# Kernel tuning notes

Hardware: AMD Instinct MI355X
Metric: run time of the kernel (lower is better)

Reference implementation:

```python
import jax, jax.numpy as jnp
import numpy as np

B, C, H, W = 32, 256, 32, 32   # batch, hidden_dim, latent grid
D, K = 256, 4096               # embedding_dim, num_embeddings
COMMITMENT_COST = 0.25


def setup_inputs() -> dict:
    key = jax.random.key(0)
    k1, k2, k3 = jax.random.split(key, 3)
    x = jax.random.normal(k1, (B, C, H, W), dtype=jnp.float32)
    conv_w = jax.random.normal(k2, (D, C), dtype=jnp.float32) * 0.02  # 1x1 conv kernel
    conv_b = jnp.zeros((D,), dtype=jnp.float32)
    # torch init: uniform_(-1/num_embeddings, 1/num_embeddings)
    emb = jax.random.uniform(k3, (K, D), dtype=jnp.float32,
                             minval=-1.0 / K, maxval=1.0 / K)
    return {"x": x, "conv_w": conv_w, "conv_b": conv_b, "emb": emb}


def reference(x, conv_w, conv_b, emb):
    # pre_vq_conv1: 1x1 conv == per-pixel matmul
    z = jnp.einsum('bchw,dc->bdhw', x, conv_w) + conv_b[None, :, None, None]
    inputs = jnp.transpose(z, (0, 2, 3, 1))            # [B,H,W,D]
    flat = inputs.reshape(-1, D)                       # [N,D]
    dist = (jnp.sum(flat * flat, axis=1, keepdims=True)
            + jnp.sum(emb * emb, axis=1)
            - 2.0 * flat @ emb.T)                      # [N,K]
    idx = jnp.argmin(dist, axis=1)                     # [N]
    # one-hot @ emb == direct gather
    quantized = emb[idx].reshape(inputs.shape)         # [B,H,W,D]
    sg = jax.lax.stop_gradient
    e_latent_loss = jnp.mean((sg(quantized) - inputs) ** 2)
    q_latent_loss = jnp.mean((quantized - sg(inputs)) ** 2)
    loss = q_latent_loss + COMMITMENT_COST * e_latent_loss
    # straight-through estimator
    quantized_st = inputs + sg(quantized - inputs)
    quantized_out = jnp.transpose(quantized_st, (0, 3, 1, 2))  # [B,D,H,W]
    # perplexity: mean one-hot == normalized code counts
    n = flat.shape[0]
    avg_probs = jnp.zeros((K,), dtype=jnp.float32).at[idx].add(1.0) / n
    perplexity = jnp.exp(-jnp.sum(avg_probs * jnp.log(avg_probs + 1e-10)))
    return quantized_out, loss, perplexity
```

## Files before the change

kernel.cpp:

```cpp
#include <hip/hip_runtime.h>
#include <math.h>

#define BB   32
#define CC   256
#define HH   32
#define WW   32
#define DD   256
#define KK   4096
#define HW   1024
#define NPIX 32768
#define NELE 8388608
#define EPS_REPAIR 1e-5f

typedef unsigned short ushort_t;
typedef __attribute__((ext_vector_type(8))) short short8;
typedef __attribute__((ext_vector_type(4))) float f32x4;

__device__ __forceinline__ unsigned short f2bf(float v) {
    union { float f; unsigned u; } c; c.f = v;
    unsigned r = c.u + 0x7FFFu + ((c.u >> 16) & 1u);
    return (unsigned short)(r >> 16);
}
__device__ __forceinline__ float bf2f(unsigned short b) {
    union { unsigned u; float f; } c; c.u = ((unsigned)b) << 16;
    return c.f;
}
__device__ __forceinline__ void gll16(const void* g, void* l) {
    __builtin_amdgcn_global_load_lds(
        (const __attribute__((address_space(1))) void*)g,
        (__attribute__((address_space(3))) void*)l, 16, 0, 0);
}

__global__ void k_zero(int* __restrict__ counts, float* __restrict__ accum) {
    int i = blockIdx.x * 256 + threadIdx.x;
    if (i < KK) counts[i] = 0;
    if (i < 2)  accum[i]  = 0.0f;
}

__global__ void k_packB(const float* __restrict__ emb, ushort_t* __restrict__ Bp,
                        float* __restrict__ e_norm) {
    int k = blockIdx.x;
    int lane = threadIdx.x;
    float4 v = reinterpret_cast<const float4*>(emb + (size_t)k * DD)[lane];
    float s = v.x * v.x + v.y * v.y + v.z * v.z + v.w * v.w;
    float vv[4] = {v.x, v.y, v.z, v.w};
    ushort_t* row = Bp + (size_t)k * 768 + lane * 4;
    #pragma unroll
    for (int c = 0; c < 4; ++c) {
        unsigned short h = f2bf(vv[c]);
        unsigned short l = f2bf(vv[c] - bf2f(h));
        row[c] = h; row[256 + c] = h; row[512 + c] = l;
    }
    #pragma unroll
    for (int off = 32; off; off >>= 1) s += __shfl_down(s, off);
    if (lane == 0) e_norm[k] = s;
}

__global__ __launch_bounds__(256) void k_conv(const float* __restrict__ x,
                                              const float* __restrict__ w,
                                              const float* __restrict__ bias,
                                              ushort_t* __restrict__ A2) {
    __shared__ __align__(16) float xt[32][260];
    int t = threadIdx.x;
    int n0 = blockIdx.x * 32;
    int b = n0 >> 10, hw0 = n0 & 1023;
    const float* xb = x + (size_t)b * (CC * HW) + hw0;

    int p = t & 31, cg = t >> 5;
    #pragma unroll
    for (int it = 0; it < 32; ++it) {
        int c = it * 8 + cg;
        xt[p][c] = xb[c * HW + p];
    }
    __syncthreads();

    int d = t;
    float acc[32];
    float bv = bias[d];
    #pragma unroll
    for (int i = 0; i < 32; ++i) acc[i] = bv;

    const float4* wrow = reinterpret_cast<const float4*>(w + (size_t)d * CC);
    for (int c4 = 0; c4 < 64; ++c4) {
        float4 w4 = wrow[c4];
        #pragma unroll
        for (int pp = 0; pp < 32; ++pp) {
            float4 x4 = *reinterpret_cast<const float4*>(&xt[pp][c4 * 4]);
            acc[pp] = fmaf(w4.x, x4.x, acc[pp]);
            acc[pp] = fmaf(w4.y, x4.y, acc[pp]);
            acc[pp] = fmaf(w4.z, x4.z, acc[pp]);
            acc[pp] = fmaf(w4.w, x4.w, acc[pp]);
        }
    }
    #pragma unroll
    for (int pp = 0; pp < 32; ++pp) {
        float v = acc[pp];
        unsigned short h = f2bf(v);
        unsigned short l = f2bf(v - bf2f(h));
        ushort_t* arow = A2 + (size_t)(n0 + pp) * 512;
        arow[d] = h; arow[256 + d] = l;
    }
}

__global__ __launch_bounds__(256, 2) void k_mfma_top2(
    const ushort_t* __restrict__ A2,
    const ushort_t* __restrict__ Bp,
    const float* __restrict__ e_norm,
    float* __restrict__ tv1, int* __restrict__ ti1,
    float* __restrict__ tv2, int* __restrict__ ti2) {
    __shared__ __align__(16) short As[128][64];
    __shared__ __align__(16) short Bs[128][64];
    __shared__ float mgv[128][2][2];
    __shared__ int   mgi[128][2][2];

    const int t  = threadIdx.x;
    const int mb = blockIdx.x >> 2, ch = blockIdx.x & 3;
    const int n0 = mb * 128, c0 = ch * 1024;
    const int w  = t >> 6, lane = t & 63;
    const int wr = w >> 1, wc = w & 1;
    const int lr = lane & 15, lg = lane >> 4;

    const int srow = t >> 3;
    const int scol = (t & 7) * 8;

    float v1[4][4], v2r[4][4];
    int   i1[4][4], i2r[4][4];
    #pragma unroll
    for (int m = 0; m < 4; ++m)
        #pragma unroll
        for (int j = 0; j < 4; ++j) {
            v1[m][j] = 3.0e38f; v2r[m][j] = 3.0e38f;
            i1[m][j] = 0x7FFFFFFF; i2r[m][j] = 0x7FFFFFFF;
        }

    for (int sub = 0; sub < 8; ++sub) {
        const int code0 = c0 + sub * 128;
        f32x4 acc[4][4];
        const f32x4 vz = {0.f, 0.f, 0.f, 0.f};
        #pragma unroll
        for (int m = 0; m < 4; ++m)
            #pragma unroll
            for (int n = 0; n < 4; ++n) acc[m][n] = vz;

        for (int ks = 0; ks < 12; ++ks) {
            const int Acol = (ks < 8) ? ks * 64 : (ks - 8) * 64;
            const int Bcol = ks * 64;
            __syncthreads();
            #pragma unroll
            for (int s = 0; s < 4; ++s) {
                const int r = srow + 32 * s;
                gll16(&A2[(size_t)(n0 + r) * 512 + Acol + scol], &As[r][scol]);
                gll16(&Bp[(size_t)(code0 + r) * 768 + Bcol + scol], &Bs[r][scol]);
            }
            __syncthreads();
            #pragma unroll
            for (int kk = 0; kk < 2; ++kk) {
                short8 a[4], b[4];
                #pragma unroll
                for (int m = 0; m < 4; ++m)
                    a[m] = *reinterpret_cast<const short8*>(
                        &As[wr * 64 + m * 16 + lr][kk * 32 + lg * 8]);
                #pragma unroll
                for (int n = 0; n < 4; ++n)
                    b[n] = *reinterpret_cast<const short8*>(
                        &Bs[wc * 64 + n * 16 + lr][kk * 32 + lg * 8]);
                #pragma unroll
                for (int m = 0; m < 4; ++m)
                    #pragma unroll
                    for (int n = 0; n < 4; ++n)
                        acc[m][n] = __builtin_amdgcn_mfma_f32_16x16x32_bf16(
                            a[m], b[n], acc[m][n], 0, 0, 0);
            }
        }
        #pragma unroll
        for (int n = 0; n < 4; ++n) {
            const int col = code0 + wc * 64 + n * 16 + lr;
            const float en = e_norm[col];
            #pragma unroll
            for (int m = 0; m < 4; ++m)
                #pragma unroll
                for (int j = 0; j < 4; ++j) {
                    const float s = fmaf(-2.0f, acc[m][n][j], en);
                    const bool b1 = s < v1[m][j];
                    const bool b2 = s < v2r[m][j];
                    v2r[m][j] = b1 ? v1[m][j] : (b2 ? s : v2r[m][j]);
                    i2r[m][j] = b1 ? i1[m][j] : (b2 ? col : i2r[m][j]);
                    v1[m][j]  = b1 ? s   : v1[m][j];
                    i1[m][j]  = b1 ? col : i1[m][j];
                }
        }
    }

    #pragma unroll
    for (int mask = 1; mask <= 8; mask <<= 1) {
        #pragma unroll
        for (int m = 0; m < 4; ++m)
            #pragma unroll
            for (int j = 0; j < 4; ++j) {
                const float ov1 = __shfl_xor(v1[m][j], mask);
                const int   oi1 = __shfl_xor(i1[m][j], mask);
                const float ov2 = __shfl_xor(v2r[m][j], mask);
                const int   oi2 = __shfl_xor(i2r[m][j], mask);
                const bool tb = (ov1 < v1[m][j]) || (ov1 == v1[m][j] && oi1 < i1[m][j]);
                const float w1 = tb ? ov1 : v1[m][j];  const int w1i = tb ? oi1 : i1[m][j];
                const float l1 = tb ? v1[m][j] : ov1;  const int l1i = tb ? i1[m][j] : oi1;
                const float c2 = tb ? ov2 : v2r[m][j]; const int c2i = tb ? oi2 : i2r[m][j];
                const bool t2b = (c2 < l1) || (c2 == l1 && c2i < l1i);
                v1[m][j] = w1; i1[m][j] = w1i;
                v2r[m][j] = t2b ? c2 : l1; i2r[m][j] = t2b ? c2i : l1i;
            }
    }
    if (lr == 0) {
        #pragma unroll
        for (int m = 0; m < 4; ++m)
            #pragma unroll
            for (int j = 0; j < 4; ++j) {
                const int r = wr * 64 + m * 16 + lg * 4 + j;
                mgv[r][wc][0] = v1[m][j];  mgv[r][wc][1] = v2r[m][j];
                mgi[r][wc][0] = i1[m][j];  mgi[r][wc][1] = i2r[m][j];
            }
    }
    __syncthreads();
    if (t < 128) {
        const float a1 = mgv[t][0][0], a2 = mgv[t][0][1];
        const int  ai1 = mgi[t][0][0], ai2 = mgi[t][0][1];
        const float b1 = mgv[t][1][0], b2 = mgv[t][1][1];
        const int  bi1 = mgi[t][1][0], bi2 = mgi[t][1][1];
        const bool tb = (b1 < a1) || (b1 == a1 && bi1 < ai1);
        const float w1 = tb ? b1 : a1;  const int w1i = tb ? bi1 : ai1;
        const float l1 = tb ? a1 : b1;  const int l1i = tb ? ai1 : bi1;
        const float c2 = tb ? b2 : a2;  const int c2i = tb ? bi2 : ai2;
        const bool t2b = (c2 < l1) || (c2 == l1 && c2i < l1i);
        const size_t o = (size_t)ch * NPIX + n0 + t;
        tv1[o] = w1; ti1[o] = w1i;
        tv2[o] = t2b ? c2 : l1; ti2[o] = t2b ? c2i : l1i;
    }
}

__global__ __launch_bounds__(256) void k_select(
    const float* __restrict__ tv1, const int* __restrict__ ti1,
    const float* __restrict__ tv2, const int* __restrict__ ti2,
    const ushort_t* __restrict__ A2, const float* __restrict__ emb,
    const float* __restrict__ e_norm, int* __restrict__ idx) {
    const int n = blockIdx.x * 256 + threadIdx.x;
    float g1 = tv1[n], g2 = tv2[n];
    int  gi1 = ti1[n], gi2 = ti2[n];
    #pragma unroll
    for (int c = 1; c < 4; ++c) {
        const size_t o = (size_t)c * NPIX + n;
        const float b1 = tv1[o], b2 = tv2[o];
        const int  bi1 = ti1[o], bi2 = ti2[o];
        const bool tb = (b1 < g1) || (b1 == g1 && bi1 < gi1);
        const float w1 = tb ? b1 : g1;  const int w1i = tb ? bi1 : gi1;
        const float l1 = tb ? g1 : b1;  const int l1i = tb ? gi1 : bi1;
        const float c2 = tb ? b2 : g2;  const int c2i = tb ? bi2 : gi2;
        const bool t2b = (c2 < l1) || (c2 == l1 && c2i < l1i);
        g1 = w1; gi1 = w1i;
        g2 = t2b ? c2 : l1; gi2 = t2b ? c2i : l1i;
    }
    int best = gi1;
    if (g2 - g1 < EPS_REPAIR) {
        const ushort_t* za = A2 + (size_t)n * 512;
        const float* e1 = emb + (size_t)gi1 * DD;
        const float* e2 = emb + (size_t)gi2 * DD;
        float d1 = 0.f, d2 = 0.f;
        for (int d = 0; d < DD; ++d) {
            const float z = bf2f(za[d]) + bf2f(za[256 + d]);
            d1 = fmaf(z, e1[d], d1);
            d2 = fmaf(z, e2[d], d2);
        }
        const float s1 = e_norm[gi1] - 2.f * d1;
        const float s2 = e_norm[gi2] - 2.f * d2;
        best = (s2 < s1 || (s2 == s1 && gi2 < gi1)) ? gi2 : gi1;
    }
    idx[n] = best;
}

__global__ __launch_bounds__(256) void k_gather(const float* __restrict__ emb,
                                                const ushort_t* __restrict__ A2,
                                                const int* __restrict__ idx,
                                                float* __restrict__ out,
                                                float* __restrict__ accum) {
    __shared__ float qt[256][33];
    int t = threadIdx.x;
    int n0 = blockIdx.x * 32;
    int b = n0 >> 10, hw0 = n0 & 1023;

    float ss = 0.0f;
    for (int p = 0; p < 32; ++p) {
        int row = idx[n0 + p];
        float q = emb[(size_t)row * DD + t];
        const ushort_t* za = A2 + (size_t)(n0 + p) * 512;
        float z = bf2f(za[t]) + bf2f(za[256 + t]);
        float df = q - z;
        ss = fmaf(df, df, ss);
        qt[t][p] = q;
    }
    __syncthreads();

    int dg = t >> 5, p = t & 31;
    float* ob = out + (size_t)b * (DD * HW) + hw0;
    #pragma unroll
    for (int s = 0; s < 32; ++s) {
        int d = dg + 8 * s;
        ob[d * HW + p] = qt[d][p];
    }

    #pragma unroll
    for (int off = 32; off; off >>= 1) ss += __shfl_down(ss, off);
    __shared__ float wsum[4];
    if ((t & 63) == 0) wsum[t >> 6] = ss;
    __syncthreads();
    if (t == 0) atomicAdd(accum, wsum[0] + wsum[1] + wsum[2] + wsum[3]);
}

__global__ void k_hist(const int* __restrict__ idx, int* __restrict__ counts) {
    int i = blockIdx.x * 256 + threadIdx.x;
    atomicAdd(&counts[idx[i]], 1);
}

__global__ void k_final(const int* __restrict__ counts, const float* __restrict__ accum,
                        float* __restrict__ out_scalars) {
    int t = threadIdx.x;
    float s = 0.0f;
    #pragma unroll
    for (int q = 0; q < 16; ++q) {
        float p = (float)counts[t * 16 + q] * (1.0f / 32768.0f);
        s += p * logf(p + 1e-10f);
    }
    #pragma unroll
    for (int off = 32; off; off >>= 1) s += __shfl_down(s, off);
    __shared__ float wsum[4];
    if ((t & 63) == 0) wsum[t >> 6] = s;
    __syncthreads();
    if (t == 0) {
        float ent = wsum[0] + wsum[1] + wsum[2] + wsum[3];
        out_scalars[0] = accum[0] * (1.25f / (float)NELE);
        out_scalars[1] = expf(-ent);
    }
}

extern "C" void kernel_launch(void* const* d_in, const int* in_sizes, int n_in,
                              void* d_out, int out_size, void* d_ws, size_t ws_size,
                              hipStream_t stream) {
    const float* x    = (const float*)d_in[0];
    const float* w    = (const float*)d_in[1];
    const float* bias = (const float*)d_in[2];
    const float* emb  = (const float*)d_in[3];
    float* out = (float*)d_out;

    char* ws = (char*)d_ws;
    ushort_t* A2   = (ushort_t*)ws;
    ushort_t* Bp   = (ushort_t*)(ws + 33554432);
    float* e_norm  = (float*)(ws + 39845888);
    int*   idx     = (int*)  (ws + 39862272);
    int*   counts  = (int*)  (ws + 39993344);
    float* accum   = (float*)(ws + 40009728);
    float* tv1     = (float*)(ws + 40009984);
    int*   ti1     = (int*)  (ws + 40534272);
    float* tv2     = (float*)(ws + 41058560);
    int*   ti2     = (int*)  (ws + 41582848);

    k_zero     <<<17,   256, 0, stream>>>(counts, accum);
    k_packB    <<<KK,    64, 0, stream>>>(emb, Bp, e_norm);
    k_conv     <<<1024, 256, 0, stream>>>(x, w, bias, A2);
    k_mfma_top2<<<1024, 256, 0, stream>>>(A2, Bp, e_norm, tv1, ti1, tv2, ti2);
    k_select   <<<128,  256, 0, stream>>>(tv1, ti1, tv2, ti2, A2, emb, e_norm, idx);
    k_gather   <<<1024, 256, 0, stream>>>(emb, A2, idx, out, accum);
    k_hist     <<<128,  256, 0, stream>>>(idx, counts);
    k_final    <<<1,    256, 0, stream>>>(counts, accum, out + NELE);
}
```

Before: 544.4 us.

## Double-buffer MFMA tiles with LDS swizzle, XCD-aware block mapping, and fuse small kernels

The main distance GEMM now double-buffers its LDS tiles, so the async global-to-LDS loads for the next k-step are issued before the current step's MFMAs. This drops one barrier per step. LDS columns are XOR-swizzled to avoid bank conflicts, and block indices are remapped so blocks sharing the same codebook chunk land on the same XCD, for better L2 reuse. The zeroing kernel is folded into packB and the histogram into select, removing two launches. The repair threshold is also tightened and the repair dot product vectorized, which may change which near-tie cases get rechecked.

```diff
diff --git a/kernel.cpp b/kernel.cpp
--- a/kernel.cpp
+++ b/kernel.cpp
@@ -3,14 +3,12 @@
 
 #define BB   32
 #define CC   256
-#define HH   32
-#define WW   32
 #define DD   256
 #define KK   4096
 #define HW   1024
 #define NPIX 32768
 #define NELE 8388608
-#define EPS_REPAIR 1e-5f
+#define EPS_REPAIR 1e-6f
 
 typedef unsigned short ushort_t;
 typedef __attribute__((ext_vector_type(8))) short short8;
@@ -31,16 +29,13 @@
         (__attribute__((address_space(3))) void*)l, 16, 0, 0);
 }
 
-__global__ void k_zero(int* __restrict__ counts, float* __restrict__ accum) {
-    int i = blockIdx.x * 256 + threadIdx.x;
-    if (i < KK) counts[i] = 0;
-    if (i < 2)  accum[i]  = 0.0f;
-}
-
 __global__ void k_packB(const float* __restrict__ emb, ushort_t* __restrict__ Bp,
-                        float* __restrict__ e_norm) {
+                        float* __restrict__ e_norm, int* __restrict__ counts,
+                        float* __restrict__ accum) {
     int k = blockIdx.x;
     int lane = threadIdx.x;
+    if (lane == 0) counts[k] = 0;
+    if (k == 0 && lane < 2) accum[lane] = 0.0f;
     float4 v = reinterpret_cast<const float4*>(emb + (size_t)k * DD)[lane];
     float s = v.x * v.x + v.y * v.y + v.z * v.z + v.w * v.w;
     float vv[4] = {v.x, v.y, v.z, v.w};
@@ -108,20 +103,23 @@
     const float* __restrict__ e_norm,
     float* __restrict__ tv1, int* __restrict__ ti1,
     float* __restrict__ tv2, int* __restrict__ ti2) {
-    __shared__ __align__(16) short As[128][64];
-    __shared__ __align__(16) short Bs[128][64];
-    __shared__ float mgv[128][2][2];
-    __shared__ int   mgi[128][2][2];
-
-    const int t  = threadIdx.x;
-    const int mb = blockIdx.x >> 2, ch = blockIdx.x & 3;
+    __shared__ __align__(16) short smem[2][2][128][64];
+
+    const int t = threadIdx.x;
+    const int xcd = blockIdx.x & 7, slot = blockIdx.x >> 3;
+    const int ch = xcd >> 1;
+    const int mb = ((xcd & 1) << 7) | slot;
     const int n0 = mb * 128, c0 = ch * 1024;
-    const int w  = t >> 6, lane = t & 63;
+    const int w = t >> 6, lane = t & 63;
     const int wr = w >> 1, wc = w & 1;
     const int lr = lane & 15, lg = lane >> 4;
 
     const int srow = t >> 3;
-    const int scol = (t & 7) * 8;
+    const int g    = t & 7;
+    const int sg   = (g ^ (srow & 7)) * 8;
+
+    const int rc0 = ((lg)     ^ (lr & 7)) * 8;
+    const int rc1 = ((4 + lg) ^ (lr & 7)) * 8;
 
     float v1[4][4], v2r[4][4];
     int   i1[4][4], i2r[4][4];
@@ -133,62 +131,76 @@
             i1[m][j] = 0x7FFFFFFF; i2r[m][j] = 0x7FFFFFFF;
         }
 
-    for (int sub = 0; sub < 8; ++sub) {
-        const int code0 = c0 + sub * 128;
-        f32x4 acc[4][4];
-        const f32x4 vz = {0.f, 0.f, 0.f, 0.f};
-        #pragma unroll
-        for (int m = 0; m < 4; ++m)
-            #pragma unroll
-            for (int n = 0; n < 4; ++n) acc[m][n] = vz;
-
-        for (int ks = 0; ks < 12; ++ks) {
-            const int Acol = (ks < 8) ? ks * 64 : (ks - 8) * 64;
-            const int Bcol = ks * 64;
-            __syncthreads();
-            #pragma unroll
-            for (int s = 0; s < 4; ++s) {
-                const int r = srow + 32 * s;
-                gll16(&A2[(size_t)(n0 + r) * 512 + Acol + scol], &As[r][scol]);
-                gll16(&Bp[(size_t)(code0 + r) * 768 + Bcol + scol], &Bs[r][scol]);
-            }
-            __syncthreads();
-            #pragma unroll
-            for (int kk = 0; kk < 2; ++kk) {
-                short8 a[4], b[4];
+    auto stage = [&](int buf, int sb, int kstep) {
+        const int code0 = c0 + sb * 128;
+        const int Acol = ((kstep < 8) ? kstep : kstep - 8) * 64;
+        const int Bcol = kstep * 64;
+        #pragma unroll
+        for (int s = 0; s < 4; ++s) {
+            const int r = srow + 32 * s;
+            gll16(&A2[(size_t)(n0 + r) * 512 + Acol + sg], &smem[buf][0][r][g * 8]);
+            gll16(&Bp[(size_t)(code0 + r) * 768 + Bcol + sg], &smem[buf][1][r][g * 8]);
+        }
+    };
+
+    f32x4 acc[4][4];
+    stage(0, 0, 0);
+    __syncthreads();
+    int cur = 0, sub = 0, ks = 0;
+    while (true) {
+        int nks = ks + 1, nsub = sub;
+        if (nks == 12) { nks = 0; nsub = sub + 1; }
+        if (nsub < 8) stage(cur ^ 1, nsub, nks);
+
+        if (ks == 0) {
+            const f32x4 vz = {0.f, 0.f, 0.f, 0.f};
+            #pragma unroll
+            for (int m = 0; m < 4; ++m)
                 #pragma unroll
-                for (int m = 0; m < 4; ++m)
-                    a[m] = *reinterpret_cast<const short8*>(
-                        &As[wr * 64 + m * 16 + lr][kk * 32 + lg * 8]);
+                for (int n = 0; n < 4; ++n) acc[m][n] = vz;
+        }
+        #pragma unroll
+        for (int kk = 0; kk < 2; ++kk) {
+            const int rc = kk ? rc1 : rc0;
+            short8 a[4], b[4];
+            #pragma unroll
+            for (int m = 0; m < 4; ++m)
+                a[m] = *reinterpret_cast<const short8*>(
+                    &smem[cur][0][wr * 64 + m * 16 + lr][rc]);
+            #pragma unroll
+            for (int n = 0; n < 4; ++n)
+                b[n] = *reinterpret_cast<const short8*>(
+                    &smem[cur][1][wc * 64 + n * 16 + lr][rc]);
+            #pragma unroll
+            for (int m = 0; m < 4; ++m)
                 #pragma unroll
                 for (int n = 0; n < 4; ++n)
-                    b[n] = *reinterpret_cast<const short8*>(
-                        &Bs[wc * 64 + n * 16 + lr][kk * 32 + lg * 8]);
+                    acc[m][n] = __builtin_amdgcn_mfma_f32_16x16x32_bf16(
+                        a[m], b[n], acc[m][n], 0, 0, 0);
+        }
+        if (ks == 11) {
+            const int code0 = c0 + sub * 128;
+            #pragma unroll
+            for (int n = 0; n < 4; ++n) {
+                const int col = code0 + wc * 64 + n * 16 + lr;
+                const float en = e_norm[col];
                 #pragma unroll
                 for (int m = 0; m < 4; ++m)
                     #pragma unroll
-                    for (int n = 0; n < 4; ++n)
-                        acc[m][n] = __builtin_amdgcn_mfma_f32_16x16x32_bf16(
-                            a[m], b[n], acc[m][n], 0, 0, 0);
+                    for (int j = 0; j < 4; ++j) {
+                        const float s = fmaf(-2.0f, acc[m][n][j], en);
+                        const bool b1 = s < v1[m][j];
+                        const bool b2 = s < v2r[m][j];
+                        v2r[m][j] = b1 ? v1[m][j] : (b2 ? s : v2r[m][j]);
+                        i2r[m][j] = b1 ? i1[m][j] : (b2 ? col : i2r[m][j]);
+                        v1[m][j]  = b1 ? s   : v1[m][j];
+                        i1[m][j]  = b1 ? col : i1[m][j];
+                    }
             }
         }
-        #pragma unroll
-        for (int n = 0; n < 4; ++n) {
-            const int col = code0 + wc * 64 + n * 16 + lr;
-            const float en = e_norm[col];
-            #pragma unroll
-            for (int m = 0; m < 4; ++m)
-                #pragma unroll
-                for (int j = 0; j < 4; ++j) {
-                    const float s = fmaf(-2.0f, acc[m][n][j], en);
-                    const bool b1 = s < v1[m][j];
-                    const bool b2 = s < v2r[m][j];
-                    v2r[m][j] = b1 ? v1[m][j] : (b2 ? s : v2r[m][j]);
-                    i2r[m][j] = b1 ? i1[m][j] : (b2 ? col : i2r[m][j]);
-                    v1[m][j]  = b1 ? s   : v1[m][j];
-                    i1[m][j]  = b1 ? col : i1[m][j];
-                }
-        }
+        __syncthreads();
+        cur ^= 1; ks = nks; sub = nsub;
+        if (sub == 8) break;
     }
 
     #pragma unroll
@@ -210,22 +222,24 @@
                 v2r[m][j] = t2b ? c2 : l1; i2r[m][j] = t2b ? c2i : l1i;
             }
     }
+    float* mgv = (float*)&smem[0][0][0][0];
+    int*   mgi = (int*)((char*)&smem[0][0][0][0] + 2048);
     if (lr == 0) {
         #pragma unroll
         for (int m = 0; m < 4; ++m)
             #pragma unroll
             for (int j = 0; j < 4; ++j) {
                 const int r = wr * 64 + m * 16 + lg * 4 + j;
-                mgv[r][wc][0] = v1[m][j];  mgv[r][wc][1] = v2r[m][j];
-                mgi[r][wc][0] = i1[m][j];  mgi[r][wc][1] = i2r[m][j];
+                mgv[(r * 2 + wc) * 2 + 0] = v1[m][j];  mgv[(r * 2 + wc) * 2 + 1] = v2r[m][j];
+                mgi[(r * 2 + wc) * 2 + 0] = i1[m][j];  mgi[(r * 2 + wc) * 2 + 1] = i2r[m][j];
             }
     }
     __syncthreads();
     if (t < 128) {
-        const float a1 = mgv[t][0][0], a2 = mgv[t][0][1];
-        const int  ai1 = mgi[t][0][0], ai2 = mgi[t][0][1];
-        const float b1 = mgv[t][1][0], b2 = mgv[t][1][1];
-        const int  bi1 = mgi[t][1][0], bi2 = mgi[t][1][1];
+        const float a1 = mgv[(t * 2 + 0) * 2 + 0], a2 = mgv[(t * 2 + 0) * 2 + 1];
+        const int  ai1 = mgi[(t * 2 + 0) * 2 + 0], ai2 = mgi[(t * 2 + 0) * 2 + 1];
+        const float b1 = mgv[(t * 2 + 1) * 2 + 0], b2 = mgv[(t * 2 + 1) * 2 + 1];
+        const int  bi1 = mgi[(t * 2 + 1) * 2 + 0], bi2 = mgi[(t * 2 + 1) * 2 + 1];
         const bool tb = (b1 < a1) || (b1 == a1 && bi1 < ai1);
         const float w1 = tb ? b1 : a1;  const int w1i = tb ? bi1 : ai1;
         const float l1 = tb ? a1 : b1;  const int l1i = tb ? ai1 : bi1;
@@ -241,7 +255,8 @@
     const float* __restrict__ tv1, const int* __restrict__ ti1,
     const float* __restrict__ tv2, const int* __restrict__ ti2,
     const ushort_t* __restrict__ A2, const float* __restrict__ emb,
-    const float* __restrict__ e_norm, int* __restrict__ idx) {
+    const float* __restrict__ e_norm, int* __restrict__ idx,
+    int* __restrict__ counts) {
     const int n = blockIdx.x * 256 + threadIdx.x;
     float g1 = tv1[n], g2 = tv2[n];
     int  gi1 = ti1[n], gi2 = ti2[n];
@@ -261,19 +276,26 @@
     int best = gi1;
     if (g2 - g1 < EPS_REPAIR) {
         const ushort_t* za = A2 + (size_t)n * 512;
-        const float* e1 = emb + (size_t)gi1 * DD;
-        const float* e2 = emb + (size_t)gi2 * DD;
+        const float4* e1 = reinterpret_cast<const float4*>(emb + (size_t)gi1 * DD);
+        const float4* e2 = reinterpret_cast<const float4*>(emb + (size_t)gi2 * DD);
         float d1 = 0.f, d2 = 0.f;
-        for (int d = 0; d < DD; ++d) {
-            const float z = bf2f(za[d]) + bf2f(za[256 + d]);
-            d1 = fmaf(z, e1[d], d1);
-            d2 = fmaf(z, e2[d], d2);
+        for (int q = 0; q < 64; ++q) {
+            const float4 a1 = e1[q], a2 = e2[q];
+            #pragma unroll
+            for (int c = 0; c < 4; ++c) {
+                const int d = q * 4 + c;
+                const float z = bf2f(za[d]) + bf2f(za[256 + d]);
+                const float ev1 = (&a1.x)[c], ev2 = (&a2.x)[c];
+                d1 = fmaf(z, ev1, d1);
+                d2 = fmaf(z, ev2, d2);
+            }
         }
         const float s1 = e_norm[gi1] - 2.f * d1;
         const float s2 = e_norm[gi2] - 2.f * d2;
         best = (s2 < s1 || (s2 == s1 && gi2 < gi1)) ? gi2 : gi1;
     }
     idx[n] = best;
+    atomicAdd(&counts[best], 1);
 }
 
 __global__ __launch_bounds__(256) void k_gather(const float* __restrict__ emb,
@@ -312,11 +334,6 @@
     if ((t & 63) == 0) wsum[t >> 6] = ss;
     __syncthreads();
     if (t == 0) atomicAdd(accum, wsum[0] + wsum[1] + wsum[2] + wsum[3]);
-}
-
-__global__ void k_hist(const int* __restrict__ idx, int* __restrict__ counts) {
-    int i = blockIdx.x * 256 + threadIdx.x;
-    atomicAdd(&counts[idx[i]], 1);
 }
 
 __global__ void k_final(const int* __restrict__ counts, const float* __restrict__ accum,
@@ -361,12 +378,10 @@
     float* tv2     = (float*)(ws + 41058560);
     int*   ti2     = (int*)  (ws + 41582848);
 
-    k_zero     <<<17,   256, 0, stream>>>(counts, accum);
-    k_packB    <<<KK,    64, 0, stream>>>(emb, Bp, e_norm);
+    k_packB    <<<KK,    64, 0, stream>>>(emb, Bp, e_norm, counts, accum);
     k_conv     <<<1024, 256, 0, stream>>>(x, w, bias, A2);
     k_mfma_top2<<<1024, 256, 0, stream>>>(A2, Bp, e_norm, tv1, ti1, tv2, ti2);
-    k_select   <<<128,  256, 0, stream>>>(tv1, ti1, tv2, ti2, A2, emb, e_norm, idx);
+    k_select   <<<128,  256, 0, stream>>>(tv1, ti1, tv2, ti2, A2, emb, e_norm, idx, counts);
     k_gather   <<<1024, 256, 0, stream>>>(emb, A2, idx, out, accum);
-    k_hist     <<<128,  256, 0, stream>>>(idx, counts);
     k_final    <<<1,    256, 0, stream>>>(counts, accum, out + NELE);
 }
```

Result: faster. 463.8 us (-14.8%).
